# Kernel optimization log

Measured on AMD Instinct MI355X. Metric: run time of the kernel, lower is better.

## Reference

```python
import jax, jax.numpy as jnp
import numpy as np

N_NODES = 100000
N_EDGES = 640000
D_IN = 128
D_OUT = 128
D_HID = 128  # assumed MLP hidden width (repo MLP not shown; standard 2-layer GIN MLP)


def setup_inputs() -> dict:
    key = jax.random.key(0)
    k = jax.random.split(key, 8)
    x = jax.random.normal(k[0], (N_NODES, D_IN), dtype=jnp.float32)
    edge_index = jax.random.randint(k[1], (2, N_EDGES), 0, N_NODES, dtype=jnp.int64)
    edge_attr = jax.random.normal(k[2], (N_EDGES, D_IN), dtype=jnp.float32)
    # learned params
    eps = jnp.zeros((), dtype=jnp.float32)  # train_eps=True, init 0
    s1 = 1.0 / np.sqrt(D_IN)
    s2 = 1.0 / np.sqrt(D_HID)
    W1 = jax.random.uniform(k[3], (D_IN, D_HID), jnp.float32, -s1, s1)
    b1 = jax.random.uniform(k[4], (D_HID,), jnp.float32, -s1, s1)
    W2 = jax.random.uniform(k[5], (D_HID, D_OUT), jnp.float32, -s2, s2)
    b2 = jax.random.uniform(k[6], (D_OUT,), jnp.float32, -s2, s2)
    return {"x": x, "edge_index": edge_index, "edge_attr": edge_attr,
            "eps": eps, "W1": W1, "b1": b1, "W2": W2, "b2": b2}


def reference(x, edge_index, edge_attr, eps, W1, b1, W2, b2):
    src = edge_index[0]  # source nodes j
    dst = edge_index[1]  # target nodes i
    # message: ReLU(x_j + edge_attr)  -- [E, D_IN]
    msg = jax.nn.relu(x[src] + edge_attr)
    # scatter-sum aggregation to target nodes -- [N, D_IN]
    aggr = jax.ops.segment_sum(msg, dst, num_segments=N_NODES)
    # GINE update: (1 + eps) * x_i + aggr, then MLP (dropout=0.0 -> identity)
    h = (1.0 + eps) * x + aggr
    h = jax.nn.relu(h @ W1 + b1)
    out = h @ W2 + b2
    return out
```

## Files before the change

kernel.cpp:

```cpp
#include <hip/hip_runtime.h>

constexpr int NN = 100000;
constexpr int NE = 640000;
constexpr int D  = 128;
constexpr int NB = (NN + 255) / 256;

typedef __attribute__((ext_vector_type(8))) short bf16x8;
typedef __attribute__((ext_vector_type(4))) float f32x4;

__device__ __forceinline__ short f2bf(float f) {
    union { float f; unsigned u; } v; v.f = f;
    unsigned r = v.u + 0x7FFF + ((v.u >> 16) & 1);
    return (short)(r >> 16);
}
__device__ __forceinline__ float bf2f(short h) {
    union { unsigned u; float f; } v;
    v.u = ((unsigned)(unsigned short)h) << 16;
    return v.f;
}

__global__ __launch_bounds__(256) void k_zero(int* __restrict__ cnt) {
    int i = blockIdx.x * 256 + threadIdx.x;
    if (i < NN) cnt[i] = 0;
}

__global__ __launch_bounds__(256) void k_hist(const int* __restrict__ dst,
                                              int* __restrict__ cnt) {
    int e = blockIdx.x * 256 + threadIdx.x;
    if (e < NE) atomicAdd(&cnt[dst[e]], 1);
}

__global__ __launch_bounds__(256) void k_bsum(const int* __restrict__ cnt,
                                              int* __restrict__ bsum) {
    int i = blockIdx.x * 256 + threadIdx.x;
    int v = (i < NN) ? cnt[i] : 0;
#pragma unroll
    for (int s = 32; s; s >>= 1) v += __shfl_down(v, s, 64);
    __shared__ int w[4];
    if ((threadIdx.x & 63) == 0) w[threadIdx.x >> 6] = v;
    __syncthreads();
    if (threadIdx.x == 0) bsum[blockIdx.x] = w[0] + w[1] + w[2] + w[3];
}

__global__ __launch_bounds__(512) void k_scan_bsum(const int* __restrict__ bsum,
                                                   int* __restrict__ bboff) {
    int t = threadIdx.x, lane = t & 63;
    int v = (t < NB) ? bsum[t] : 0;
    int incl = v;
#pragma unroll
    for (int s = 1; s < 64; s <<= 1) {
        int u = __shfl_up(incl, s, 64);
        if (lane >= s) incl += u;
    }
    __shared__ int wt[8], wp[8];
    if (lane == 63) wt[t >> 6] = incl;
    __syncthreads();
    if (t == 0) { int run = 0; for (int i = 0; i < 8; ++i) { wp[i] = run; run += wt[i]; } }
    __syncthreads();
    if (t < NB) bboff[t] = incl - v + wp[t >> 6];
}

__global__ __launch_bounds__(256) void k_scan_final(const int* __restrict__ cnt,
                                                    const int* __restrict__ bboff,
                                                    int* __restrict__ off,
                                                    int* __restrict__ cur) {
    int b = blockIdx.x, t = threadIdx.x, lane = t & 63;
    int i = b * 256 + t;
    int v = (i < NN) ? cnt[i] : 0;
    int incl = v;
#pragma unroll
    for (int s = 1; s < 64; s <<= 1) {
        int u = __shfl_up(incl, s, 64);
        if (lane >= s) incl += u;
    }
    __shared__ int wt[4], wp[4];
    if (lane == 63) wt[t >> 6] = incl;
    __syncthreads();
    if (t == 0) { int run = 0; for (int q = 0; q < 4; ++q) { wp[q] = run; run += wt[q]; } }
    __syncthreads();
    int excl = incl - v + wp[t >> 6] + bboff[b];
    if (i < NN) { off[i] = excl; cur[i] = excl; }
    if (i == 0) off[NN] = NE;
}

__global__ __launch_bounds__(256) void k_perm(const int* __restrict__ dst,
                                              const int* __restrict__ src,
                                              int* __restrict__ cur,
                                              int2* __restrict__ ps) {
    int e = blockIdx.x * 256 + threadIdx.x;
    if (e < NE) {
        int p = atomicAdd(&cur[dst[e]], 1);
        int2 v; v.x = e; v.y = src[e];
        ps[p] = v;
    }
}

__global__ __launch_bounds__(256) void k_wsplit(const float* __restrict__ W,
                                                short* __restrict__ Whi,
                                                short* __restrict__ Wlo) {
    for (int idx = blockIdx.x * 256 + threadIdx.x; idx < D * D; idx += gridDim.x * 256) {
        int n = idx >> 7, k = idx & 127;
        float w = W[k * D + n];
        short hi = f2bf(w);
        Whi[idx] = hi;
        Wlo[idx] = f2bf(w - bf2f(hi));
    }
}

__global__ __launch_bounds__(256) void k_agg(const float* __restrict__ x,
                                             const float* __restrict__ ea,
                                             const int* __restrict__ off,
                                             const int2* __restrict__ ps,
                                             const float* __restrict__ eps,
                                             float* __restrict__ h) {
    int wave = threadIdx.x >> 6;
    int lane = threadIdx.x & 63;
    int n = blockIdx.x * 4 + wave;
    if (n >= NN) return;
    int j0 = off[n], j1 = off[n + 1];
    const int lo2 = lane * 2;
    float2 acc; acc.x = 0.0f; acc.y = 0.0f;

    for (int j = j0; j < j1; j += 8) {
        int ee[8], ss[8];
#pragma unroll
        for (int q = 0; q < 8; ++q) {
            int jj = j + q; jj = (jj < j1) ? jj : (j1 - 1);
            int2 p = ps[jj];
            ee[q] = p.x; ss[q] = p.y;
        }
        float2 xa[8], eb[8];
#pragma unroll
        for (int q = 0; q < 8; ++q) {
            xa[q] = *reinterpret_cast<const float2*>(x  + (size_t)ss[q] * D + lo2);
            eb[q] = *reinterpret_cast<const float2*>(ea + (size_t)ee[q] * D + lo2);
        }
#pragma unroll
        for (int q = 0; q < 8; ++q) {
            float mx = fmaxf(xa[q].x + eb[q].x, 0.0f);
            float my = fmaxf(xa[q].y + eb[q].y, 0.0f);
            bool ok = (j + q) < j1;
            acc.x += ok ? mx : 0.0f;
            acc.y += ok ? my : 0.0f;
        }
    }
    float sc = 1.0f + eps[0];
    float2 xx = *reinterpret_cast<const float2*>(x + (size_t)n * D + lo2);
    float2 o;
    o.x = fmaf(sc, xx.x, acc.x);
    o.y = fmaf(sc, xx.y, acc.y);
    *reinterpret_cast<float2*>(h + (size_t)n * D + lo2) = o;
}

__global__ __launch_bounds__(256) void k_mlp2(const float* __restrict__ A,
                                              const short* __restrict__ W1h,
                                              const short* __restrict__ W1l,
                                              const short* __restrict__ W2h,
                                              const short* __restrict__ W2l,
                                              const float* __restrict__ b1,
                                              const float* __restrict__ b2,
                                              float* __restrict__ out) {
    __shared__ float G[4][32][D];

    const int wave = threadIdx.x >> 6;
    const int lane = threadIdx.x & 63;
    const int r = lane & 15;
    const int g = lane >> 4;

    const long rb = (long)blockIdx.x * 128 + wave * 32;

    f32x4 acc1[2][8];
#pragma unroll
    for (int mt = 0; mt < 2; ++mt)
#pragma unroll
        for (int nt = 0; nt < 8; ++nt) {
            acc1[mt][nt].x = 0.f; acc1[mt][nt].y = 0.f;
            acc1[mt][nt].z = 0.f; acc1[mt][nt].w = 0.f;
        }

#pragma unroll
    for (int kc = 0; kc < 4; ++kc) {
        const int k0 = kc * 32;
        bf16x8 ahi[2], alo[2];
#pragma unroll
        for (int mt = 0; mt < 2; ++mt) {
            long row = rb + mt * 16 + r;
            row = (row < NN) ? row : (NN - 1);
            const float* ap = A + row * D + k0 + g * 8;
            float4 v0 = reinterpret_cast<const float4*>(ap)[0];
            float4 v1 = reinterpret_cast<const float4*>(ap)[1];
            float vals[8] = {v0.x, v0.y, v0.z, v0.w, v1.x, v1.y, v1.z, v1.w};
#pragma unroll
            for (int i = 0; i < 8; ++i) {
                short hb = f2bf(vals[i]);
                ahi[mt][i] = hb;
                alo[mt][i] = f2bf(vals[i] - bf2f(hb));
            }
        }
#pragma unroll
        for (int nt = 0; nt < 8; ++nt) {
            const int wb = (nt * 16 + r) * D + k0 + g * 8;
            bf16x8 whi = *reinterpret_cast<const bf16x8*>(&W1h[wb]);
            bf16x8 wlo = *reinterpret_cast<const bf16x8*>(&W1l[wb]);
#pragma unroll
            for (int mt = 0; mt < 2; ++mt) {
                acc1[mt][nt] = __builtin_amdgcn_mfma_f32_16x16x32_bf16(ahi[mt], whi, acc1[mt][nt], 0, 0, 0);
                acc1[mt][nt] = __builtin_amdgcn_mfma_f32_16x16x32_bf16(ahi[mt], wlo, acc1[mt][nt], 0, 0, 0);
                acc1[mt][nt] = __builtin_amdgcn_mfma_f32_16x16x32_bf16(alo[mt], whi, acc1[mt][nt], 0, 0, 0);
            }
        }
    }

#pragma unroll
    for (int nt = 0; nt < 8; ++nt) {
        const int col = nt * 16 + r;
        const float bb = b1[col];
#pragma unroll
        for (int mt = 0; mt < 2; ++mt) {
#pragma unroll
            for (int q = 0; q < 4; ++q) {
                float v = fmaxf(acc1[mt][nt][q] + bb, 0.0f);
                G[wave][mt * 16 + g * 4 + q][col] = v;
            }
        }
    }
    __syncthreads();

    f32x4 acc2[2][8];
#pragma unroll
    for (int mt = 0; mt < 2; ++mt)
#pragma unroll
        for (int nt = 0; nt < 8; ++nt) {
            acc2[mt][nt].x = 0.f; acc2[mt][nt].y = 0.f;
            acc2[mt][nt].z = 0.f; acc2[mt][nt].w = 0.f;
        }

#pragma unroll
    for (int kc = 0; kc < 4; ++kc) {
        const int k0 = kc * 32;
        bf16x8 ahi[2], alo[2];
#pragma unroll
        for (int mt = 0; mt < 2; ++mt) {
            const float* gp = &G[wave][mt * 16 + r][k0 + g * 8];
            float4 v0 = reinterpret_cast<const float4*>(gp)[0];
            float4 v1 = reinterpret_cast<const float4*>(gp)[1];
            float vals[8] = {v0.x, v0.y, v0.z, v0.w, v1.x, v1.y, v1.z, v1.w};
#pragma unroll
            for (int i = 0; i < 8; ++i) {
                short hb = f2bf(vals[i]);
                ahi[mt][i] = hb;
                alo[mt][i] = f2bf(vals[i] - bf2f(hb));
            }
        }
#pragma unroll
        for (int nt = 0; nt < 8; ++nt) {
            const int wb = (nt * 16 + r) * D + k0 + g * 8;
            bf16x8 whi = *reinterpret_cast<const bf16x8*>(&W2h[wb]);
            bf16x8 wlo = *reinterpret_cast<const bf16x8*>(&W2l[wb]);
#pragma unroll
            for (int mt = 0; mt < 2; ++mt) {
                acc2[mt][nt] = __builtin_amdgcn_mfma_f32_16x16x32_bf16(ahi[mt], whi, acc2[mt][nt], 0, 0, 0);
                acc2[mt][nt] = __builtin_amdgcn_mfma_f32_16x16x32_bf16(ahi[mt], wlo, acc2[mt][nt], 0, 0, 0);
                acc2[mt][nt] = __builtin_amdgcn_mfma_f32_16x16x32_bf16(alo[mt], whi, acc2[mt][nt], 0, 0, 0);
            }
        }
    }

#pragma unroll
    for (int nt = 0; nt < 8; ++nt) {
        const int col = nt * 16 + r;
        const float bb = b2[col];
#pragma unroll
        for (int mt = 0; mt < 2; ++mt) {
#pragma unroll
            for (int q = 0; q < 4; ++q) {
                long row = rb + mt * 16 + g * 4 + q;
                if (row < NN) out[row * D + col] = acc2[mt][nt][q] + bb;
            }
        }
    }
}

extern "C" void kernel_launch(void* const* d_in, const int* in_sizes, int n_in,
                              void* d_out, int out_size, void* d_ws, size_t ws_size,
                              hipStream_t stream) {
    const float* x   = (const float*)d_in[0];
    const int*   ei  = (const int*)d_in[1];
    const float* ea  = (const float*)d_in[2];
    const float* eps = (const float*)d_in[3];
    const float* W1  = (const float*)d_in[4];
    const float* b1  = (const float*)d_in[5];
    const float* W2  = (const float*)d_in[6];
    const float* b2  = (const float*)d_in[7];
    float* out = (float*)d_out;

    const int* src = ei;
    const int* dst = ei + NE;

    int* base  = (int*)d_ws;
    int* cnt   = base;
    int* off   = cnt + NN;
    int* cur   = off + NN + 1;
    int* bsum  = cur + NN;
    int* bboff = bsum + NB;
    size_t ps_off = ((size_t)(3 * NN + 1 + 2 * NB) + 1) & ~(size_t)1;
    int2* ps   = (int2*)(base + ps_off);
    short* wsp = (short*)(base + ps_off + 2 * (size_t)NE);
    short* W1h = wsp;
    short* W1l = W1h + D * D;
    short* W2h = W1l + D * D;
    short* W2l = W2h + D * D;

    k_wsplit    <<<32,               256, 0, stream>>>(W1, W1h, W1l);
    k_wsplit    <<<32,               256, 0, stream>>>(W2, W2h, W2l);
    k_zero      <<<NB,               256, 0, stream>>>(cnt);
    k_hist      <<<(NE + 255) / 256, 256, 0, stream>>>(dst, cnt);
    k_bsum      <<<NB,               256, 0, stream>>>(cnt, bsum);
    k_scan_bsum <<<1,                512, 0, stream>>>(bsum, bboff);
    k_scan_final<<<NB,               256, 0, stream>>>(cnt, bboff, off, cur);
    k_perm      <<<(NE + 255) / 256, 256, 0, stream>>>(dst, src, cur, ps);

    k_agg<<<(NN + 3) / 4, 256, 0, stream>>>(x, ea, off, ps, eps, out);
    k_mlp2<<<(NN + 127) / 128, 256, 0, stream>>>(out, W1h, W1l, W2h, W2l, b1, b2, out);
}
```

Baseline: 304.6 us.

## Materialize per-edge bf16 messages in CSR order, then aggregate contiguously

Messages are now computed in a separate edge-parallel kernel. It reads edge_attr rows sequentially in original edge order, applies ReLU(x_src + ea) and writes the result as bf16 into a buffer at the edge's CSR position. The aggregation kernel then streams contiguous bf16 rows per destination node instead of gathering edge_attr rows randomly. This removes the random 512-byte edge_attr gathers but adds a 164MB intermediate write and read. Rounding messages to bf16 also adds precision loss in the sum.

```diff
diff --git a/kernel.cpp b/kernel.cpp
--- a/kernel.cpp
+++ b/kernel.cpp
@@ -83,16 +83,11 @@
     if (i == 0) off[NN] = NE;
 }
 
-__global__ __launch_bounds__(256) void k_perm(const int* __restrict__ dst,
-                                              const int* __restrict__ src,
-                                              int* __restrict__ cur,
-                                              int2* __restrict__ ps) {
+__global__ __launch_bounds__(256) void k_pos(const int* __restrict__ dst,
+                                             int* __restrict__ cur,
+                                             int* __restrict__ pos) {
     int e = blockIdx.x * 256 + threadIdx.x;
-    if (e < NE) {
-        int p = atomicAdd(&cur[dst[e]], 1);
-        int2 v; v.x = e; v.y = src[e];
-        ps[p] = v;
-    }
+    if (e < NE) pos[e] = atomicAdd(&cur[dst[e]], 1);
 }
 
 __global__ __launch_bounds__(256) void k_wsplit(const float* __restrict__ W,
@@ -107,48 +102,62 @@
     }
 }
 
-__global__ __launch_bounds__(256) void k_agg(const float* __restrict__ x,
+__global__ __launch_bounds__(256) void k_msg(const float* __restrict__ x,
+                                             const int* __restrict__ src,
                                              const float* __restrict__ ea,
-                                             const int* __restrict__ off,
-                                             const int2* __restrict__ ps,
-                                             const float* __restrict__ eps,
-                                             float* __restrict__ h) {
+                                             const int* __restrict__ pos,
+                                             unsigned short* __restrict__ mbuf) {
+    unsigned gid = blockIdx.x * 256 + threadIdx.x;
+    unsigned e = gid >> 4;
+    unsigned c = gid & 15;
+    const int s = src[e];
+    const int p = pos[e];
+    const float* eap = ea + (size_t)e * D + c * 8;
+    const float* xp  = x  + (size_t)s * D + c * 8;
+    float4 a0 = reinterpret_cast<const float4*>(xp)[0];
+    float4 a1 = reinterpret_cast<const float4*>(xp)[1];
+    float4 b0 = reinterpret_cast<const float4*>(eap)[0];
+    float4 b1 = reinterpret_cast<const float4*>(eap)[1];
+    float m[8] = {a0.x + b0.x, a0.y + b0.y, a0.z + b0.z, a0.w + b0.w,
+                  a1.x + b1.x, a1.y + b1.y, a1.z + b1.z, a1.w + b1.w};
+    bf16x8 o;
+#pragma unroll
+    for (int i = 0; i < 8; ++i) o[i] = f2bf(fmaxf(m[i], 0.0f));
+    *reinterpret_cast<bf16x8*>(mbuf + (size_t)p * D + c * 8) = o;
+}
+
+__global__ __launch_bounds__(256) void k_agg2(const float* __restrict__ x,
+                                              const unsigned short* __restrict__ mbuf,
+                                              const int* __restrict__ off,
+                                              const float* __restrict__ eps,
+                                              float* __restrict__ h) {
     int wave = threadIdx.x >> 6;
     int lane = threadIdx.x & 63;
     int n = blockIdx.x * 4 + wave;
     if (n >= NN) return;
     int j0 = off[n], j1 = off[n + 1];
     const int lo2 = lane * 2;
-    float2 acc; acc.x = 0.0f; acc.y = 0.0f;
-
-    for (int j = j0; j < j1; j += 8) {
-        int ee[8], ss[8];
-#pragma unroll
-        for (int q = 0; q < 8; ++q) {
+    float accx = 0.0f, accy = 0.0f;
+
+    for (int j = j0; j < j1; j += 4) {
+        ushort2 mv[4];
+#pragma unroll
+        for (int q = 0; q < 4; ++q) {
             int jj = j + q; jj = (jj < j1) ? jj : (j1 - 1);
-            int2 p = ps[jj];
-            ee[q] = p.x; ss[q] = p.y;
-        }
-        float2 xa[8], eb[8];
-#pragma unroll
-        for (int q = 0; q < 8; ++q) {
-            xa[q] = *reinterpret_cast<const float2*>(x  + (size_t)ss[q] * D + lo2);
-            eb[q] = *reinterpret_cast<const float2*>(ea + (size_t)ee[q] * D + lo2);
-        }
-#pragma unroll
-        for (int q = 0; q < 8; ++q) {
-            float mx = fmaxf(xa[q].x + eb[q].x, 0.0f);
-            float my = fmaxf(xa[q].y + eb[q].y, 0.0f);
+            mv[q] = *reinterpret_cast<const ushort2*>(mbuf + (size_t)jj * D + lo2);
+        }
+#pragma unroll
+        for (int q = 0; q < 4; ++q) {
             bool ok = (j + q) < j1;
-            acc.x += ok ? mx : 0.0f;
-            acc.y += ok ? my : 0.0f;
+            accx += ok ? bf2f((short)mv[q].x) : 0.0f;
+            accy += ok ? bf2f((short)mv[q].y) : 0.0f;
         }
     }
     float sc = 1.0f + eps[0];
     float2 xx = *reinterpret_cast<const float2*>(x + (size_t)n * D + lo2);
     float2 o;
-    o.x = fmaf(sc, xx.x, acc.x);
-    o.y = fmaf(sc, xx.y, acc.y);
+    o.x = fmaf(sc, xx.x, accx);
+    o.y = fmaf(sc, xx.y, accy);
     *reinterpret_cast<float2*>(h + (size_t)n * D + lo2) = o;
 }
 
@@ -303,9 +312,10 @@
     int* cur   = off + NN + 1;
     int* bsum  = cur + NN;
     int* bboff = bsum + NB;
-    size_t ps_off = ((size_t)(3 * NN + 1 + 2 * NB) + 1) & ~(size_t)1;
-    int2* ps   = (int2*)(base + ps_off);
-    short* wsp = (short*)(base + ps_off + 2 * (size_t)NE);
+    int* pos   = bboff + NB;
+    size_t mb_off = ((size_t)(3 * NN + 1 + 2 * NB + NE) + 63) & ~(size_t)63;
+    unsigned short* mbuf = (unsigned short*)(base + mb_off);
+    short* wsp = (short*)(mbuf + (size_t)NE * D);
     short* W1h = wsp;
     short* W1l = W1h + D * D;
     short* W2h = W1l + D * D;
@@ -318,8 +328,9 @@
     k_bsum      <<<NB,               256, 0, stream>>>(cnt, bsum);
     k_scan_bsum <<<1,                512, 0, stream>>>(bsum, bboff);
     k_scan_final<<<NB,               256, 0, stream>>>(cnt, bboff, off, cur);
-    k_perm      <<<(NE + 255) / 256, 256, 0, stream>>>(dst, src, cur, ps);
-
-    k_agg<<<(NN + 3) / 4, 256, 0, stream>>>(x, ea, off, ps, eps, out);
+    k_pos       <<<(NE + 255) / 256, 256, 0, stream>>>(dst, cur, pos);
+
+    k_msg <<<NE * 16 / 256, 256, 0, stream>>>(x, src, ea, pos, mbuf);
+    k_agg2<<<(NN + 3) / 4, 256, 0, stream>>>(x, mbuf, off, eps, out);
     k_mlp2<<<(NN + 127) / 128, 256, 0, stream>>>(out, W1h, W1l, W2h, W2l, b1, b2, out);
 }
```

After: 323.0 us. 6.0% more time.

## Fuse aggregation and MLP into one kernel with LDS-staged tiles

Applied to the files above, without the earlier changes.

Merges the edge aggregation and the two-layer MLP into one kernel. Each block aggregates 32 nodes into shared memory, then runs both GEMMs from shared memory, so the intermediate h never makes a global-memory round trip. The MFMA work is now split across waves by output columns, and the LDS rows are padded to avoid bank conflicts. Packed bf16 conversion intrinsics replace the manual rounding, and the second GEMM drops the low-part activation term, which lowers accuracy there. The grid assumes NN is divisible by 32 and removes the row bounds checks.

```diff
diff --git a/kernel.cpp b/kernel.cpp
--- a/kernel.cpp
+++ b/kernel.cpp
@@ -1,4 +1,5 @@
 #include <hip/hip_runtime.h>
+#include <hip/hip_bf16.h>
 
 constexpr int NN = 100000;
 constexpr int NE = 640000;
@@ -17,6 +18,31 @@
     union { unsigned u; float f; } v;
     v.u = ((unsigned)(unsigned short)h) << 16;
     return v.f;
+}
+__device__ __forceinline__ unsigned cvtpk(float a, float b) {
+    union { __hip_bfloat162 h2; unsigned u; } cv;
+    float2 f; f.x = a; f.y = b;
+    cv.h2 = __float22bfloat162_rn(f);
+    return cv.u;
+}
+__device__ __forceinline__ void pack_hilo(const float* v, bf16x8& hi, bf16x8& lo) {
+#pragma unroll
+    for (int i = 0; i < 4; ++i) {
+        unsigned u = cvtpk(v[2 * i], v[2 * i + 1]);
+        short h0 = (short)(u & 0xFFFF), h1 = (short)(u >> 16);
+        hi[2 * i] = h0; hi[2 * i + 1] = h1;
+        unsigned ul = cvtpk(v[2 * i] - bf2f(h0), v[2 * i + 1] - bf2f(h1));
+        lo[2 * i] = (short)(ul & 0xFFFF); lo[2 * i + 1] = (short)(ul >> 16);
+    }
+}
+__device__ __forceinline__ bf16x8 pack_bf8(const float* v) {
+    bf16x8 o;
+#pragma unroll
+    for (int i = 0; i < 4; ++i) {
+        unsigned u = cvtpk(v[2 * i], v[2 * i + 1]);
+        o[2 * i] = (short)(u & 0xFFFF); o[2 * i + 1] = (short)(u >> 16);
+    }
+    return o;
 }
 
 __global__ __launch_bounds__(256) void k_zero(int* __restrict__ cnt) {
@@ -107,176 +133,166 @@
     }
 }
 
-__global__ __launch_bounds__(256) void k_agg(const float* __restrict__ x,
-                                             const float* __restrict__ ea,
-                                             const int* __restrict__ off,
-                                             const int2* __restrict__ ps,
-                                             const float* __restrict__ eps,
-                                             float* __restrict__ h) {
-    int wave = threadIdx.x >> 6;
-    int lane = threadIdx.x & 63;
-    int n = blockIdx.x * 4 + wave;
-    if (n >= NN) return;
-    int j0 = off[n], j1 = off[n + 1];
-    const int lo2 = lane * 2;
-    float2 acc; acc.x = 0.0f; acc.y = 0.0f;
-
-    for (int j = j0; j < j1; j += 8) {
-        int ee[8], ss[8];
-#pragma unroll
-        for (int q = 0; q < 8; ++q) {
-            int jj = j + q; jj = (jj < j1) ? jj : (j1 - 1);
-            int2 p = ps[jj];
-            ee[q] = p.x; ss[q] = p.y;
-        }
-        float2 xa[8], eb[8];
-#pragma unroll
-        for (int q = 0; q < 8; ++q) {
-            xa[q] = *reinterpret_cast<const float2*>(x  + (size_t)ss[q] * D + lo2);
-            eb[q] = *reinterpret_cast<const float2*>(ea + (size_t)ee[q] * D + lo2);
-        }
-#pragma unroll
-        for (int q = 0; q < 8; ++q) {
-            float mx = fmaxf(xa[q].x + eb[q].x, 0.0f);
-            float my = fmaxf(xa[q].y + eb[q].y, 0.0f);
-            bool ok = (j + q) < j1;
-            acc.x += ok ? mx : 0.0f;
-            acc.y += ok ? my : 0.0f;
-        }
-    }
-    float sc = 1.0f + eps[0];
-    float2 xx = *reinterpret_cast<const float2*>(x + (size_t)n * D + lo2);
-    float2 o;
-    o.x = fmaf(sc, xx.x, acc.x);
-    o.y = fmaf(sc, xx.y, acc.y);
-    *reinterpret_cast<float2*>(h + (size_t)n * D + lo2) = o;
-}
-
-__global__ __launch_bounds__(256) void k_mlp2(const float* __restrict__ A,
-                                              const short* __restrict__ W1h,
-                                              const short* __restrict__ W1l,
-                                              const short* __restrict__ W2h,
-                                              const short* __restrict__ W2l,
-                                              const float* __restrict__ b1,
-                                              const float* __restrict__ b2,
-                                              float* __restrict__ out) {
-    __shared__ float G[4][32][D];
+constexpr int LDG = 132;
+
+__global__ __launch_bounds__(256) void k_fused(const float* __restrict__ x,
+                                               const float* __restrict__ ea,
+                                               const int* __restrict__ off,
+                                               const int2* __restrict__ ps,
+                                               const float* __restrict__ eps,
+                                               const short* __restrict__ W1h,
+                                               const short* __restrict__ W1l,
+                                               const short* __restrict__ W2h,
+                                               const short* __restrict__ W2l,
+                                               const float* __restrict__ b1,
+                                               const float* __restrict__ b2,
+                                               float* __restrict__ out) {
+    __shared__ float G1[32 * LDG];
+    __shared__ float G2[32 * LDG];
 
     const int wave = threadIdx.x >> 6;
     const int lane = threadIdx.x & 63;
+    const int nb = blockIdx.x * 32;
+
+    {
+        const int lo2 = lane * 2;
+        const float sc = 1.0f + eps[0];
+        for (int t = 0; t < 8; ++t) {
+            const int n = nb + wave * 8 + t;
+            const int j0 = off[n], j1 = off[n + 1];
+            float accx = 0.0f, accy = 0.0f;
+            for (int j = j0; j < j1; j += 8) {
+                int ee[8], ss[8];
+#pragma unroll
+                for (int q = 0; q < 8; ++q) {
+                    int jj = j + q; jj = (jj < j1) ? jj : (j1 - 1);
+                    int2 p = ps[jj];
+                    ee[q] = p.x; ss[q] = p.y;
+                }
+                float2 xa[8], eb[8];
+#pragma unroll
+                for (int q = 0; q < 8; ++q) {
+                    xa[q] = *reinterpret_cast<const float2*>(x  + (size_t)ss[q] * D + lo2);
+                    eb[q] = *reinterpret_cast<const float2*>(ea + (size_t)ee[q] * D + lo2);
+                }
+#pragma unroll
+                for (int q = 0; q < 8; ++q) {
+                    float mx = fmaxf(xa[q].x + eb[q].x, 0.0f);
+                    float my = fmaxf(xa[q].y + eb[q].y, 0.0f);
+                    bool ok = (j + q) < j1;
+                    accx += ok ? mx : 0.0f;
+                    accy += ok ? my : 0.0f;
+                }
+            }
+            float2 xx = *reinterpret_cast<const float2*>(x + (size_t)n * D + lo2);
+            float2 o;
+            o.x = fmaf(sc, xx.x, accx);
+            o.y = fmaf(sc, xx.y, accy);
+            *reinterpret_cast<float2*>(&G1[(wave * 8 + t) * LDG + lo2]) = o;
+        }
+    }
+    __syncthreads();
+
     const int r = lane & 15;
     const int g = lane >> 4;
 
-    const long rb = (long)blockIdx.x * 128 + wave * 32;
-
-    f32x4 acc1[2][8];
-#pragma unroll
-    for (int mt = 0; mt < 2; ++mt)
-#pragma unroll
-        for (int nt = 0; nt < 8; ++nt) {
-            acc1[mt][nt].x = 0.f; acc1[mt][nt].y = 0.f;
-            acc1[mt][nt].z = 0.f; acc1[mt][nt].w = 0.f;
-        }
-
-#pragma unroll
-    for (int kc = 0; kc < 4; ++kc) {
-        const int k0 = kc * 32;
-        bf16x8 ahi[2], alo[2];
-#pragma unroll
-        for (int mt = 0; mt < 2; ++mt) {
-            long row = rb + mt * 16 + r;
-            row = (row < NN) ? row : (NN - 1);
-            const float* ap = A + row * D + k0 + g * 8;
-            float4 v0 = reinterpret_cast<const float4*>(ap)[0];
-            float4 v1 = reinterpret_cast<const float4*>(ap)[1];
-            float vals[8] = {v0.x, v0.y, v0.z, v0.w, v1.x, v1.y, v1.z, v1.w};
-#pragma unroll
-            for (int i = 0; i < 8; ++i) {
-                short hb = f2bf(vals[i]);
-                ahi[mt][i] = hb;
-                alo[mt][i] = f2bf(vals[i] - bf2f(hb));
-            }
-        }
-#pragma unroll
-        for (int nt = 0; nt < 8; ++nt) {
-            const int wb = (nt * 16 + r) * D + k0 + g * 8;
-            bf16x8 whi = *reinterpret_cast<const bf16x8*>(&W1h[wb]);
-            bf16x8 wlo = *reinterpret_cast<const bf16x8*>(&W1l[wb]);
+    {
+        f32x4 acc[2][2];
+#pragma unroll
+        for (int mt = 0; mt < 2; ++mt)
+#pragma unroll
+            for (int nl = 0; nl < 2; ++nl) {
+                acc[mt][nl].x = 0.f; acc[mt][nl].y = 0.f;
+                acc[mt][nl].z = 0.f; acc[mt][nl].w = 0.f;
+            }
+
+#pragma unroll
+        for (int kc = 0; kc < 4; ++kc) {
+            const int k0 = kc * 32;
+            bf16x8 ahi[2], alo[2];
 #pragma unroll
             for (int mt = 0; mt < 2; ++mt) {
-                acc1[mt][nt] = __builtin_amdgcn_mfma_f32_16x16x32_bf16(ahi[mt], whi, acc1[mt][nt], 0, 0, 0);
-                acc1[mt][nt] = __builtin_amdgcn_mfma_f32_16x16x32_bf16(ahi[mt], wlo, acc1[mt][nt], 0, 0, 0);
-                acc1[mt][nt] = __builtin_amdgcn_mfma_f32_16x16x32_bf16(alo[mt], whi, acc1[mt][nt], 0, 0, 0);
-            }
-        }
-    }
-
-#pragma unroll
-    for (int nt = 0; nt < 8; ++nt) {
-        const int col = nt * 16 + r;
-        const float bb = b1[col];
-#pragma unroll
-        for (int mt = 0; mt < 2; ++mt) {
-#pragma unroll
-            for (int q = 0; q < 4; ++q) {
-                float v = fmaxf(acc1[mt][nt][q] + bb, 0.0f);
-                G[wave][mt * 16 + g * 4 + q][col] = v;
-            }
-        }
-    }
-    __syncthreads();
-
-    f32x4 acc2[2][8];
-#pragma unroll
-    for (int mt = 0; mt < 2; ++mt)
-#pragma unroll
-        for (int nt = 0; nt < 8; ++nt) {
-            acc2[mt][nt].x = 0.f; acc2[mt][nt].y = 0.f;
-            acc2[mt][nt].z = 0.f; acc2[mt][nt].w = 0.f;
-        }
-
-#pragma unroll
-    for (int kc = 0; kc < 4; ++kc) {
-        const int k0 = kc * 32;
-        bf16x8 ahi[2], alo[2];
-#pragma unroll
-        for (int mt = 0; mt < 2; ++mt) {
-            const float* gp = &G[wave][mt * 16 + r][k0 + g * 8];
-            float4 v0 = reinterpret_cast<const float4*>(gp)[0];
-            float4 v1 = reinterpret_cast<const float4*>(gp)[1];
-            float vals[8] = {v0.x, v0.y, v0.z, v0.w, v1.x, v1.y, v1.z, v1.w};
-#pragma unroll
-            for (int i = 0; i < 8; ++i) {
-                short hb = f2bf(vals[i]);
-                ahi[mt][i] = hb;
-                alo[mt][i] = f2bf(vals[i] - bf2f(hb));
-            }
-        }
-#pragma unroll
-        for (int nt = 0; nt < 8; ++nt) {
-            const int wb = (nt * 16 + r) * D + k0 + g * 8;
-            bf16x8 whi = *reinterpret_cast<const bf16x8*>(&W2h[wb]);
-            bf16x8 wlo = *reinterpret_cast<const bf16x8*>(&W2l[wb]);
+                const float* gp = &G1[(mt * 16 + r) * LDG + k0 + g * 8];
+                float vals[8];
+                *reinterpret_cast<float4*>(&vals[0]) = reinterpret_cast<const float4*>(gp)[0];
+                *reinterpret_cast<float4*>(&vals[4]) = reinterpret_cast<const float4*>(gp)[1];
+                pack_hilo(vals, ahi[mt], alo[mt]);
+            }
+#pragma unroll
+            for (int nl = 0; nl < 2; ++nl) {
+                const int nt = wave * 2 + nl;
+                const int wb = (nt * 16 + r) * D + k0 + g * 8;
+                bf16x8 whi = *reinterpret_cast<const bf16x8*>(&W1h[wb]);
+                bf16x8 wlo = *reinterpret_cast<const bf16x8*>(&W1l[wb]);
+#pragma unroll
+                for (int mt = 0; mt < 2; ++mt) {
+                    acc[mt][nl] = __builtin_amdgcn_mfma_f32_16x16x32_bf16(ahi[mt], whi, acc[mt][nl], 0, 0, 0);
+                    acc[mt][nl] = __builtin_amdgcn_mfma_f32_16x16x32_bf16(ahi[mt], wlo, acc[mt][nl], 0, 0, 0);
+                    acc[mt][nl] = __builtin_amdgcn_mfma_f32_16x16x32_bf16(alo[mt], whi, acc[mt][nl], 0, 0, 0);
+                }
+            }
+        }
+
+#pragma unroll
+        for (int nl = 0; nl < 2; ++nl) {
+            const int col = (wave * 2 + nl) * 16 + r;
+            const float bb = b1[col];
+#pragma unroll
+            for (int mt = 0; mt < 2; ++mt)
+#pragma unroll
+                for (int q = 0; q < 4; ++q)
+                    G2[(mt * 16 + g * 4 + q) * LDG + col] = fmaxf(acc[mt][nl][q] + bb, 0.0f);
+        }
+    }
+    __syncthreads();
+
+    {
+        f32x4 acc[2][2];
+#pragma unroll
+        for (int mt = 0; mt < 2; ++mt)
+#pragma unroll
+            for (int nl = 0; nl < 2; ++nl) {
+                acc[mt][nl].x = 0.f; acc[mt][nl].y = 0.f;
+                acc[mt][nl].z = 0.f; acc[mt][nl].w = 0.f;
+            }
+
+#pragma unroll
+        for (int kc = 0; kc < 4; ++kc) {
+            const int k0 = kc * 32;
+            bf16x8 a[2];
 #pragma unroll
             for (int mt = 0; mt < 2; ++mt) {
-                acc2[mt][nt] = __builtin_amdgcn_mfma_f32_16x16x32_bf16(ahi[mt], whi, acc2[mt][nt], 0, 0, 0);
-                acc2[mt][nt] = __builtin_amdgcn_mfma_f32_16x16x32_bf16(ahi[mt], wlo, acc2[mt][nt], 0, 0, 0);
-                acc2[mt][nt] = __builtin_amdgcn_mfma_f32_16x16x32_bf16(alo[mt], whi, acc2[mt][nt], 0, 0, 0);
-            }
-        }
-    }
-
-#pragma unroll
-    for (int nt = 0; nt < 8; ++nt) {
-        const int col = nt * 16 + r;
-        const float bb = b2[col];
-#pragma unroll
-        for (int mt = 0; mt < 2; ++mt) {
-#pragma unroll
-            for (int q = 0; q < 4; ++q) {
-                long row = rb + mt * 16 + g * 4 + q;
-                if (row < NN) out[row * D + col] = acc2[mt][nt][q] + bb;
-            }
+                const float* gp = &G2[(mt * 16 + r) * LDG + k0 + g * 8];
+                float vals[8];
+                *reinterpret_cast<float4*>(&vals[0]) = reinterpret_cast<const float4*>(gp)[0];
+                *reinterpret_cast<float4*>(&vals[4]) = reinterpret_cast<const float4*>(gp)[1];
+                a[mt] = pack_bf8(vals);
+            }
+#pragma unroll
+            for (int nl = 0; nl < 2; ++nl) {
+                const int nt = wave * 2 + nl;
+                const int wb = (nt * 16 + r) * D + k0 + g * 8;
+                bf16x8 whi = *reinterpret_cast<const bf16x8*>(&W2h[wb]);
+                bf16x8 wlo = *reinterpret_cast<const bf16x8*>(&W2l[wb]);
+#pragma unroll
+                for (int mt = 0; mt < 2; ++mt) {
+                    acc[mt][nl] = __builtin_amdgcn_mfma_f32_16x16x32_bf16(a[mt], whi, acc[mt][nl], 0, 0, 0);
+                    acc[mt][nl] = __builtin_amdgcn_mfma_f32_16x16x32_bf16(a[mt], wlo, acc[mt][nl], 0, 0, 0);
+                }
+            }
+        }
+
+#pragma unroll
+        for (int nl = 0; nl < 2; ++nl) {
+            const int col = (wave * 2 + nl) * 16 + r;
+            const float bb = b2[col];
+#pragma unroll
+            for (int mt = 0; mt < 2; ++mt)
+#pragma unroll
+                for (int q = 0; q < 4; ++q) {
+                    long row = nb + mt * 16 + g * 4 + q;
+                    out[row * D + col] = acc[mt][nl][q] + bb;
+                }
         }
     }
 }
@@ -320,6 +336,6 @@
     k_scan_final<<<NB,               256, 0, stream>>>(cnt, bboff, off, cur);
     k_perm      <<<(NE + 255) / 256, 256, 0, stream>>>(dst, src, cur, ps);
 
-    k_agg<<<(NN + 3) / 4, 256, 0, stream>>>(x, ea, off, ps, eps, out);
-    k_mlp2<<<(NN + 127) / 128, 256, 0, stream>>>(out, W1h, W1l, W2h, W2l, b1, b2, out);
-}
+    k_fused<<<NN / 32, 256, 0, stream>>>(x, ea, off, ps, eps,
+                                         W1h, W1l, W2h, W2l, b1, b2, out);
+}
```

Measured after the change: 265.3 us. -12.9%, faster.
